# Performance work log

Measured on AMD Instinct MI355X. Metric: run time of the kernel, lower is better.

Reference implementation:

```python
import jax, jax.numpy as jnp
from jax import lax
import numpy as np

B, H, W = 512, 96, 96
KH = KW = 25
PI = 3.141592653589793


def compute_ellipticity(images, counter_target=100, thr=1e-3):
    # images: [B, H, W]
    b, h, w = images.shape
    yv = jnp.arange(h, dtype=jnp.float32) - h / 2.0 + 0.5
    xv = jnp.arange(w, dtype=jnp.float32) - w / 2.0 + 0.5
    Y, X = jnp.meshgrid(yv, xv, indexing='ij')
    X = X[None]  # [1,H,W]
    Y = Y[None]
    area = jnp.float32(h * w)
    total = jnp.sum(images, axis=(1, 2))  # [B]

    init = (jnp.int32(0),
            jnp.full((b,), 3.0, jnp.float32),   # alphax
            jnp.full((b,), 3.0, jnp.float32),   # alphay
            jnp.zeros((b,), jnp.float32),       # alphaxy
            jnp.zeros((b,), jnp.float32),       # mux
            jnp.zeros((b,), jnp.float32),       # muy
            jnp.full((b,), 9999.0, jnp.float32),  # prev_sigxx
            jnp.full((b,), 9999.0, jnp.float32),  # prev_sigyy
            jnp.zeros((b,), jnp.float32),       # curr_sigxx
            jnp.zeros((b,), jnp.float32),       # curr_sigyy
            jnp.zeros((b,), jnp.float32),       # back
            jnp.zeros((b,), jnp.float32),       # e1
            jnp.zeros((b,), jnp.float32))       # e2

    def cond(c):
        i, ax, ay, axy, mux, muy, psxx, psyy, csxx, csyy, back, e1, e2 = c
        first = i == 0
        conv = ((jnp.max(jnp.abs(csxx - psxx)) < thr)
                & (jnp.max(jnp.abs(csyy - psyy)) < thr)
                & jnp.logical_not(first))
        return (i < counter_target) & (first | jnp.logical_not(conv))

    def body(c):
        i, ax, ay, axy, mux, muy, psxx, psyy, csxx, csyy, back, e1, e2 = c
        Xc = X - mux[:, None, None]
        Yc = Y - muy[:, None, None]
        rho = jnp.clip(axy / (ax * ay + 1e-10), -0.99, 0.99)
        arb = jnp.maximum(2.0 * (1.0 - rho ** 2), 1e-10)
        A = 1.0 / (2.0 * PI * ax * ay * jnp.sqrt(1.0 - rho ** 2))
        exp_term = (Xc ** 2 / (arb * ax ** 2)[:, None, None]
                    + Yc ** 2 / (arb * ay ** 2)[:, None, None]
                    - 2.0 * axy[:, None, None] * Xc * Yc
                    / (arb * ax ** 2 * ay ** 2)[:, None, None])
        k = A[:, None, None] * jnp.exp(-jnp.clip(exp_term, 0.0, 50.0))
        img1 = images - back[:, None, None]
        wk = img1 * k
        t1 = jnp.sum(X * Y * wk, axis=(1, 2))
        t2 = jnp.sum(wk, axis=(1, 2))
        t3 = jnp.sum(X * wk, axis=(1, 2))
        t4 = jnp.sum(Y * wk, axis=(1, 2))
        t5 = jnp.sum(X * X * wk, axis=(1, 2))
        t6 = jnp.sum(Y * Y * wk, axis=(1, 2))
        t7 = jnp.sum(k * k, axis=(1, 2))
        flux = t2 / (t7 + 1e-10)
        new_back = (total - flux) / area
        t2s = jnp.maximum(t2, 1e-10)
        new_mux = t3 / t2s
        new_muy = t4 / t2s
        sigxx = t5 / t2s - (t3 / t2s) ** 2
        sigyy = t6 / t2s - (t4 / t2s) ** 2
        sigxy = t1 / t2s - t3 * t4 / (t2s * t2s)
        new_ax = jnp.sqrt(jnp.clip(sigxx * 2.0, 0.81, 100.0))
        new_ay = jnp.sqrt(jnp.clip(sigyy * 2.0, 0.81, 100.0))
        new_axy = 2.0 * sigxy
        den = sigxx + sigyy + 1e-10
        new_e1 = jnp.clip((sigxx - sigyy) / den, -0.99, 0.99)
        new_e2 = jnp.clip(2.0 * sigxy / den, -0.99, 0.99)
        return (i + 1, new_ax, new_ay, new_axy, new_mux, new_muy,
                csxx, csyy, sigxx, sigyy, new_back, new_e1, new_e2)

    final = lax.while_loop(cond, body, init)
    e1, e2 = final[11], final[12]
    e1 = jnp.where(jnp.isnan(e1), 0.0, e1)
    e2 = jnp.where(jnp.isnan(e2), 0.0, e2)
    return e1, e2


def blur_with_kernel(image, kernel):
    # image: [B,H,W,1], kernel: [B,kH,kW,1]; per-sample normalized SAME conv.
    b, h, w, _ = image.shape
    ker = kernel / (jnp.sum(kernel, axis=(1, 2, 3), keepdims=True) + 1e-6)
    img = jnp.transpose(image, (0, 3, 1, 2)).reshape(1, b, h, w)  # batch -> channels
    k = jnp.transpose(ker, (0, 3, 1, 2))                          # [B,1,kH,kW] OIHW
    out = lax.conv_general_dilated(
        img, k, window_strides=(1, 1), padding='SAME',
        feature_group_count=b,
        dimension_numbers=('NCHW', 'OIHW', 'NCHW'))
    return out.reshape(b, 1, h, w).transpose(0, 2, 3, 1)


def percentile_per_sample(t, q):
    # per-sample percentile over axes [1,2,3], keepdims, gather-by-round index
    b = t.shape[0]
    flat = t.reshape(b, -1)
    n = flat.shape[-1]
    kidx = int(round(q / 100.0 * (n - 1)))
    s = jnp.sort(flat, axis=-1)
    return s[:, kidx].reshape(b, 1, 1, 1)


def loss_fn(blurred_img, kernel_img, weight_map, y_true, y_pred):
    weighted_mse = jnp.mean(jnp.square(y_pred - y_true) * weight_map)
    e1_t, e2_t = compute_ellipticity(jnp.squeeze(y_true, -1))
    e1_p, e2_p = compute_ellipticity(jnp.squeeze(y_pred, -1))
    ellip_loss = jnp.mean((e1_t - e1_p) ** 2 + (e2_t - e2_p) ** 2)
    reblurred_raw = blur_with_kernel(y_pred, kernel_img)
    vmin = percentile_per_sample(blurred_img, 1.0)
    vmax = percentile_per_sample(blurred_img, 99.0)
    scale = vmax - vmin + 1e-6
    reblurred = jnp.clip((reblurred_raw - vmin) / scale, 0.0, 2.0)
    reblur_loss = jnp.mean(jnp.square(reblurred - blurred_img) * weight_map)
    total_loss = 100.0 * weighted_mse + 10.0 * reblur_loss
    return total_loss, weighted_mse, ellip_loss, reblur_loss


def setup_inputs() -> dict:
    key = jax.random.key(0)
    ks = jax.random.split(key, 5)
    return {
        'blurred_img': jax.random.uniform(ks[0], (B, H, W, 1), jnp.float32),
        'kernel_img': jax.random.uniform(ks[1], (B, KH, KW, 1), jnp.float32),
        'weight_map': jax.random.uniform(ks[2], (B, H, W, 1), jnp.float32),
        'y_true': jax.random.uniform(ks[3], (B, H, W, 1), jnp.float32),
        'y_pred': jax.random.uniform(ks[4], (B, H, W, 1), jnp.float32),
    }


def reference(blurred_img, kernel_img, weight_map, y_true, y_pred):
    return loss_fn(blurred_img, kernel_img, weight_map, y_true, y_pred)
```

## Files before the change

kernel.cpp:

```cpp
#include <hip/hip_runtime.h>

typedef unsigned int uint32;

#define HW 9216
#define NBATCH 512
#define NPAIR 1024
#define NITER 100
#define TWO_PI_F 6.28318530717958647692f


__device__ __forceinline__ float block_reduce_sum(float v, float* lds) {
#pragma unroll
  for (int m = 1; m < 64; m <<= 1) v += __shfl_xor(v, m, 64);
  __syncthreads();
  if ((threadIdx.x & 63) == 0) lds[threadIdx.x >> 6] = v;
  __syncthreads();
  if (threadIdx.x == 0) {
    int nw = blockDim.x >> 6;
    for (int w = 1; w < nw; ++w) v += lds[w];
  }
  return v;
}


__global__ void init_kernel(double* acc) {
  if (threadIdx.x < 2) acc[threadIdx.x] = 0.0;
}


__global__ void totals_kernel(const float* __restrict__ yt, const float* __restrict__ yp,
                              float* __restrict__ totals) {
  __shared__ float lds[4];
  int pair = blockIdx.x;
  const float* img = (pair < NBATCH) ? (yt + (size_t)pair * HW)
                                     : (yp + (size_t)(pair - NBATCH) * HW);
  float s = 0.f;
  for (int j = threadIdx.x; j < HW; j += 256) s += img[j];
  s = block_reduce_sum(s, lds);
  if (threadIdx.x == 0) totals[pair] = s;
}


__device__ float radix_select(const float* __restrict__ img, int rank,
                              uint32* bins, uint32* selb) {
  uint32 prefix = 0;
  int r = rank;
#pragma unroll 1
  for (int pass = 0; pass < 4; ++pass) {
    int shift = 24 - 8 * pass;
    uint32 maskhi = (pass == 0) ? 0u : (0xFFFFFFFFu << (shift + 8));
    bins[threadIdx.x] = 0;
    __syncthreads();
    for (int j = 0; j < 36; ++j) {
      int px = threadIdx.x + j * 256;
      uint32 bits = __float_as_uint(img[px]);
      uint32 key = (bits & 0x80000000u) ? ~bits : (bits | 0x80000000u);
      if ((key & maskhi) == prefix)
        atomicAdd(&bins[(key >> shift) & 255u], 1u);
    }
    __syncthreads();
    uint32 c = bins[threadIdx.x];
    for (int d = 1; d < 256; d <<= 1) {
      uint32 v = (threadIdx.x >= (unsigned)d) ? bins[threadIdx.x - d] : 0u;
      __syncthreads();
      bins[threadIdx.x] += v;
      __syncthreads();
    }
    uint32 inc = bins[threadIdx.x];
    if (inc > (uint32)r && (inc - c) <= (uint32)r) {
      selb[0] = threadIdx.x;
      selb[1] = (uint32)r - (inc - c);
    }
    __syncthreads();
    prefix |= (selb[0] << shift);
    r = (int)selb[1];
    __syncthreads();
  }
  uint32 key = prefix;
  uint32 bits = (key & 0x80000000u) ? (key ^ 0x80000000u) : ~key;
  return __uint_as_float(bits);
}

__global__ void percentile_kernel(const float* __restrict__ blurred,
                                  float* __restrict__ vmin, float* __restrict__ vmax) {
  __shared__ uint32 bins[256];
  __shared__ uint32 selb[2];
  int b = blockIdx.x;
  const float* img = blurred + (size_t)b * HW;
  float lo = radix_select(img, 92, bins, selb);
  float hi = radix_select(img, 9123, bins, selb);
  if (threadIdx.x == 0) { vmin[b] = lo; vmax[b] = hi; }
}


__global__ void wmse_kernel(const float4* __restrict__ yt, const float4* __restrict__ yp,
                            const float4* __restrict__ wm, double* acc) {
  __shared__ float lds[4];
  int idx = blockIdx.x * 256 + threadIdx.x;
  int stride = gridDim.x * 256;
  float s = 0.f;
  for (int i = idx; i < (NBATCH * HW / 4); i += stride) {
    float4 a = yp[i], b = yt[i], w = wm[i];
    float d;
    d = a.x - b.x; s = fmaf(d * d, w.x, s);
    d = a.y - b.y; s = fmaf(d * d, w.y, s);
    d = a.z - b.z; s = fmaf(d * d, w.z, s);
    d = a.w - b.w; s = fmaf(d * d, w.w, s);
  }
  s = block_reduce_sum(s, lds);
  if (threadIdx.x == 0) atomicAdd(&acc[0], (double)s);
}


__device__ __forceinline__ void accum_row(float* a, const float fr[28], const float* krow) {
  float kv[28];
#pragma unroll
  for (int q = 0; q < 7; ++q) {
    float4 t = *reinterpret_cast<const float4*>(krow + 4 * q);
    kv[4 * q + 0] = t.x; kv[4 * q + 1] = t.y; kv[4 * q + 2] = t.z; kv[4 * q + 3] = t.w;
  }
#pragma unroll
  for (int dx = 0; dx < 25; ++dx) {
    a[0] = fmaf(fr[dx + 0], kv[dx], a[0]);
    a[1] = fmaf(fr[dx + 1], kv[dx], a[1]);
    a[2] = fmaf(fr[dx + 2], kv[dx], a[2]);
    a[3] = fmaf(fr[dx + 3], kv[dx], a[3]);
  }
}

__global__ __launch_bounds__(256, 2) void conv_kernel(
    const float* __restrict__ yp, const float* __restrict__ ker,
    const float* __restrict__ blurred, const float* __restrict__ wmap,
    const float* __restrict__ vminA, const float* __restrict__ vmaxA,
    double* acc) {
  __shared__ float pad[120 * 120];
  __shared__ float kr[25 * 28];
  __shared__ float lds[4];
  __shared__ float sInv;
  int b = blockIdx.x, tid = threadIdx.x;

  const float* kg = ker + (size_t)b * 625;
  float ks = 0.f;
  for (int i = tid; i < 700; i += 256) {
    int r = i / 28, c = i - r * 28;
    float v = (c < 25) ? kg[r * 25 + c] : 0.f;
    kr[i] = v;
    ks += v;
  }
  float ksum = block_reduce_sum(ks, lds);
  if (tid == 0) sInv = 1.f / (ksum + 1e-6f);

  const float* ig = yp + (size_t)b * HW;
  for (int i = tid; i < 14400; i += 256) {
    int r = i / 120, c = i - r * 120;
    float v = 0.f;
    if (r >= 12 && r < 108 && c >= 12 && c < 108) v = ig[(r - 12) * 96 + (c - 12)];
    pad[i] = v;
  }
  __syncthreads();

  float inv = sInv;
  float vmn = vminA[b], vmx = vmaxA[b];
  float scale = vmx - vmn + 1e-6f;
  const float* bl = blurred + (size_t)b * HW;
  const float* wm = wmap + (size_t)b * HW;

  float part = 0.f;
#pragma unroll 1
  for (int t3 = 0; t3 < 3; ++t3) {
    int tile = tid + t3 * 256;
    int ty = tile / 24, tx = tile - ty * 24;
    int y0 = ty * 3, x0 = tx * 4;
    float a0[4] = {0, 0, 0, 0}, a1[4] = {0, 0, 0, 0}, a2[4] = {0, 0, 0, 0};
#pragma unroll 1
    for (int ir = 0; ir < 27; ++ir) {
      float fr[28];
      const float* rp = &pad[(y0 + ir) * 120 + x0];
#pragma unroll
      for (int q = 0; q < 7; ++q) {
        float4 t = *reinterpret_cast<const float4*>(rp + 4 * q);
        fr[4 * q + 0] = t.x; fr[4 * q + 1] = t.y; fr[4 * q + 2] = t.z; fr[4 * q + 3] = t.w;
      }
      if (ir <= 24)            accum_row(a0, fr, &kr[ir * 28]);
      if (ir >= 1 && ir <= 25) accum_row(a1, fr, &kr[(ir - 1) * 28]);
      if (ir >= 2)             accum_row(a2, fr, &kr[(ir - 2) * 28]);
    }
    {
      const float* aa = a0;
#pragma unroll
      for (int r = 0; r < 3; ++r) {
        aa = (r == 0) ? a0 : ((r == 1) ? a1 : a2);
#pragma unroll
        for (int j = 0; j < 4; ++j) {
          int px = (y0 + r) * 96 + x0 + j;
          float raw = aa[j] * inv;
          float rb2 = fminf(fmaxf((raw - vmn) / scale, 0.f), 2.f);
          float d = rb2 - bl[px];
          part = fmaf(d * d, wm[px], part);
        }
      }
    }
  }
  part = block_reduce_sum(part, lds);
  if (tid == 0) atomicAdd(&acc[1], (double)part);
}


__global__ __launch_bounds__(256, 4) void ellipA_kernel(
    const float* __restrict__ yt, const float* __restrict__ yp,
    const float* __restrict__ totals,
    float* __restrict__ dxx, float* __restrict__ dyy,
    float* __restrict__ e1a, float* __restrict__ e2a) {
  const int pair = blockIdx.x;
  const int tid = threadIdx.x;
  const float* img = (pair < NBATCH) ? (yt + (size_t)pair * HW)
                                     : (yp + (size_t)(pair - NBATCH) * HW);
  float im[36];
#pragma unroll
  for (int j = 0; j < 36; ++j) im[j] = img[tid + j * 256];

  __shared__ float bc[8];
  __shared__ float rbuf[28];
  __shared__ int sfroz;

  float ax = 3.f, ay = 3.f, axy = 0.f, mux = 0.f, muy = 0.f, back = 0.f;
  float psxx = 0.f, psyy = 0.f;
  float total = 0.f;
  if (tid == 0) {
    total = totals[pair];
    sfroz = 0;
    float rho = fminf(fmaxf(axy / (ax * ay + 1e-10f), -0.99f), 0.99f);
    float arb = fmaxf(2.f * (1.f - rho * rho), 1e-10f);
    float Ac = 1.f / (TWO_PI_F * ax * ay * sqrtf(1.f - rho * rho));
    bc[0] = mux; bc[1] = muy; bc[2] = back; bc[3] = Ac;
    bc[4] = 1.f / (arb * ax * ax);
    bc[5] = 1.f / (arb * ay * ay);
    bc[6] = -2.f * axy / (arb * ax * ax * ay * ay);
  }
  __syncthreads();

#pragma unroll 1
  for (int n = 0; n < NITER; ++n) {
    float bmux = bc[0], bmuy = bc[1], bback = bc[2], Ac = bc[3];
    float c1 = bc[4], c2 = bc[5], c3 = bc[6];
    float s0 = 0, sx = 0, sy = 0, sxx = 0, syy = 0, sxy = 0, s7 = 0;
    int x = tid % 96, y = tid / 96;
#pragma unroll
    for (int j = 0; j < 36; ++j) {
      float Xc = ((float)x - 47.5f) - bmux;
      float Yc = ((float)y - 47.5f) - bmuy;
      float xc2 = Xc * Xc, yc2 = Yc * Yc, xy = Xc * Yc;
      float t = fmaf(c1, xc2, fmaf(c2, yc2, c3 * xy));
      t = fminf(fmaxf(t, 0.f), 50.f);
      float e = __expf(-t);
      float ge = (im[j] - bback) * e;
      s0 += ge;
      sx = fmaf(Xc, ge, sx);
      sy = fmaf(Yc, ge, sy);
      sxx = fmaf(xc2, ge, sxx);
      syy = fmaf(yc2, ge, syy);
      sxy = fmaf(xy, ge, sxy);
      s7 = fmaf(e, e, s7);
      x += 64;
      if (x >= 96) { x -= 96; y += 3; } else { y += 2; }
    }
#pragma unroll
    for (int m = 1; m < 64; m <<= 1) {
      s0 += __shfl_xor(s0, m, 64);  sx += __shfl_xor(sx, m, 64);
      sy += __shfl_xor(sy, m, 64);  sxx += __shfl_xor(sxx, m, 64);
      syy += __shfl_xor(syy, m, 64); sxy += __shfl_xor(sxy, m, 64);
      s7 += __shfl_xor(s7, m, 64);
    }
    if ((tid & 63) == 0) {
      float* p = &rbuf[(tid >> 6) * 7];
      p[0] = s0; p[1] = sx; p[2] = sy; p[3] = sxx; p[4] = syy; p[5] = sxy; p[6] = s7;
    }
    __syncthreads();
    if (tid == 0) {
      for (int w2 = 1; w2 < 4; ++w2) {
        const float* p = &rbuf[w2 * 7];
        s0 += p[0]; sx += p[1]; sy += p[2]; sxx += p[3]; syy += p[4]; sxy += p[5]; s7 += p[6];
      }
      float t2 = Ac * s0;
      float t3 = Ac * fmaf(bmux, s0, sx);
      float t4 = Ac * fmaf(bmuy, s0, sy);
      float t5 = Ac * (sxx + 2.f * bmux * sx + bmux * bmux * s0);
      float t6 = Ac * (syy + 2.f * bmuy * sy + bmuy * bmuy * s0);
      float t1 = Ac * (sxy + bmux * sy + bmuy * sx + bmux * bmuy * s0);
      float t7 = Ac * Ac * s7;
      float flux = t2 / (t7 + 1e-10f);
      float back_n = (total - flux) / 9216.f;
      float t2s = fmaxf(t2, 1e-10f);
      float mux_n = t3 / t2s, muy_n = t4 / t2s;
      float sigxx = t5 / t2s - mux_n * mux_n;
      float sigyy = t6 / t2s - muy_n * muy_n;
      float sigxy = t1 / t2s - (t3 * t4) / (t2s * t2s);
      float ax_n = sqrtf(fminf(fmaxf(sigxx * 2.f, 0.81f), 100.f));
      float ay_n = sqrtf(fminf(fmaxf(sigyy * 2.f, 0.81f), 100.f));
      float axy_n = 2.f * sigxy;
      float den = sigxx + sigyy + 1e-10f;
      float e1 = fminf(fmaxf((sigxx - sigyy) / den, -0.99f), 0.99f);
      float e2 = fminf(fmaxf((2.f * sigxy) / den, -0.99f), 0.99f);
      float dx_v = fabsf(sigxx - psxx);
      float dy_v = fabsf(sigyy - psyy);
      if (!(dx_v == dx_v)) dx_v = __int_as_float(0x7f800000);
      if (!(dy_v == dy_v)) dy_v = __int_as_float(0x7f800000);
      dxx[n * NPAIR + pair] = dx_v;
      dyy[n * NPAIR + pair] = dy_v;
      e1a[n * NPAIR + pair] = e1;
      e2a[n * NPAIR + pair] = e2;
      bool froz = (ax_n == ax) && (ay_n == ay) && (axy_n == axy) &&
                  (mux_n == mux) && (muy_n == muy) && (back_n == back) &&
                  (dx_v == 0.f) && (dy_v == 0.f);
      psxx = sigxx; psyy = sigyy;
      ax = ax_n; ay = ay_n; axy = axy_n; mux = mux_n; muy = muy_n; back = back_n;
      if (froz) {
        for (int m2 = n + 1; m2 < NITER; ++m2) {
          dxx[m2 * NPAIR + pair] = 0.f;
          dyy[m2 * NPAIR + pair] = 0.f;
          e1a[m2 * NPAIR + pair] = e1;
          e2a[m2 * NPAIR + pair] = e2;
        }
        sfroz = 1;
      } else {
        float rho = fminf(fmaxf(axy / (ax * ay + 1e-10f), -0.99f), 0.99f);
        float arb = fmaxf(2.f * (1.f - rho * rho), 1e-10f);
        float Ac2 = 1.f / (TWO_PI_F * ax * ay * sqrtf(1.f - rho * rho));
        bc[0] = mux; bc[1] = muy; bc[2] = back; bc[3] = Ac2;
        bc[4] = 1.f / (arb * ax * ax);
        bc[5] = 1.f / (arb * ay * ay);
        bc[6] = -2.f * axy / (arb * ax * ax * ay * ay);
      }
    }
    __syncthreads();
    if (sfroz) break;
  }
}


__global__ void ellipB_kernel(const float* __restrict__ dxx, const float* __restrict__ dyy,
                              const float* __restrict__ e1a, const float* __restrict__ e2a,
                              float* __restrict__ out_ellip) {
  __shared__ float rb[8];
  __shared__ int found;
  __shared__ int eidx_sh[2];
  __shared__ float lds[4];
  const int tid = threadIdx.x;

  for (int s = 0; s < 2; ++s) {
    if (tid == 0) { eidx_sh[s] = NITER - 1; found = 0; }
    __syncthreads();
#pragma unroll 1
    for (int n = 0; n < NITER - 1; ++n) {
      int base = n * NPAIR + s * NBATCH;
      float m1 = fmaxf(dxx[base + tid], dxx[base + tid + 256]);
      float m2 = fmaxf(dyy[base + tid], dyy[base + tid + 256]);
#pragma unroll
      for (int m = 1; m < 64; m <<= 1) {
        m1 = fmaxf(m1, __shfl_xor(m1, m, 64));
        m2 = fmaxf(m2, __shfl_xor(m2, m, 64));
      }
      if ((tid & 63) == 0) { rb[(tid >> 6) * 2] = m1; rb[(tid >> 6) * 2 + 1] = m2; }
      __syncthreads();
      if (tid == 0) {
        float M1 = fmaxf(fmaxf(rb[0], rb[2]), fmaxf(rb[4], rb[6]));
        float M2 = fmaxf(fmaxf(rb[1], rb[3]), fmaxf(rb[5], rb[7]));
        if (M1 < 1e-3f && M2 < 1e-3f) { eidx_sh[s] = n; found = 1; }
      }
      __syncthreads();
      if (found) break;
    }
    __syncthreads();
  }

  int i0 = eidx_sh[0], i1 = eidx_sh[1];
  float part = 0.f;
  for (int b = tid; b < NBATCH; b += 256) {
    float e1t = e1a[i0 * NPAIR + b];
    float e2t = e2a[i0 * NPAIR + b];
    float e1p = e1a[i1 * NPAIR + NBATCH + b];
    float e2p = e2a[i1 * NPAIR + NBATCH + b];
    if (!(e1t == e1t)) e1t = 0.f;
    if (!(e2t == e2t)) e2t = 0.f;
    if (!(e1p == e1p)) e1p = 0.f;
    if (!(e2p == e2p)) e2p = 0.f;
    float d1 = e1t - e1p, d2 = e2t - e2p;
    part += d1 * d1 + d2 * d2;
  }
  part = block_reduce_sum(part, lds);
  if (tid == 0) out_ellip[0] = part / (float)NBATCH;
}


__global__ void final_kernel(const double* acc, const float* ellip, float* out) {
  if (threadIdx.x == 0) {
    const double N = 4718592.0;
    float wm = (float)(acc[0] / N);
    float rb = (float)(acc[1] / N);
    out[0] = 100.f * wm + 10.f * rb;
    out[1] = wm;
    out[2] = ellip[0];
    out[3] = rb;
  }
}


extern "C" void kernel_launch(void* const* d_in, const int* in_sizes, int n_in,
                              void* d_out, int out_size, void* d_ws, size_t ws_size,
                              hipStream_t stream) {
  const float* blurred = (const float*)d_in[0];
  const float* kernel_img = (const float*)d_in[1];
  const float* wmap = (const float*)d_in[2];
  const float* y_true = (const float*)d_in[3];
  const float* y_pred = (const float*)d_in[4];
  float* out = (float*)d_out;

  double* acc = (double*)d_ws;
  float* wsf = (float*)d_ws;
  float* ellip = wsf + 4;
  float* vmin = wsf + 8;
  float* vmax = vmin + NBATCH;
  float* totals = vmax + NBATCH;
  float* dxx = totals + NPAIR;
  float* dyy = dxx + NITER * NPAIR;
  float* e1a = dyy + NITER * NPAIR;
  float* e2a = e1a + NITER * NPAIR;

  init_kernel<<<1, 64, 0, stream>>>(acc);
  totals_kernel<<<NPAIR, 256, 0, stream>>>(y_true, y_pred, totals);
  percentile_kernel<<<NBATCH, 256, 0, stream>>>(blurred, vmin, vmax);
  wmse_kernel<<<1024, 256, 0, stream>>>((const float4*)y_true, (const float4*)y_pred,
                                        (const float4*)wmap, acc);
  conv_kernel<<<NBATCH, 256, 0, stream>>>(y_pred, kernel_img, blurred, wmap, vmin, vmax, acc);
  ellipA_kernel<<<NPAIR, 256, 0, stream>>>(y_true, y_pred, totals, dxx, dyy, e1a, e2a);
  ellipB_kernel<<<1, 256, 0, stream>>>(dxx, dyy, e1a, e2a, ellip);
  final_kernel<<<1, 64, 0, stream>>>(acc, ellip, out);
}
```

Measured before the change: 1.198 ms.

## Fuse image totals into ellipse kernel and replicate per-iteration scalar update

Removes the separate totals kernel and computes each image's sum inside the ellipse-fitting kernel from the registers it already loaded. The per-iteration scalar update, previously done by thread 0 and broadcast through shared memory with a second barrier, is now computed redundantly by every thread from double-buffered wave partials, so each iteration needs one barrier instead of two. The per-iteration output arrays move to a pair-major layout to match the new writes, and the reduction kernel is updated for that layout. In exchange, every thread does the scalar math with divisions and sqrt, and the reduction kernel's reads become strided.

```diff
diff --git a/kernel.cpp b/kernel.cpp
--- a/kernel.cpp
+++ b/kernel.cpp
@@ -25,19 +25,6 @@
 
 __global__ void init_kernel(double* acc) {
   if (threadIdx.x < 2) acc[threadIdx.x] = 0.0;
-}
-
-
-__global__ void totals_kernel(const float* __restrict__ yt, const float* __restrict__ yp,
-                              float* __restrict__ totals) {
-  __shared__ float lds[4];
-  int pair = blockIdx.x;
-  const float* img = (pair < NBATCH) ? (yt + (size_t)pair * HW)
-                                     : (yp + (size_t)(pair - NBATCH) * HW);
-  float s = 0.f;
-  for (int j = threadIdx.x; j < HW; j += 256) s += img[j];
-  s = block_reduce_sum(s, lds);
-  if (threadIdx.x == 0) totals[pair] = s;
 }
 
 
@@ -208,7 +195,6 @@
 
 __global__ __launch_bounds__(256, 4) void ellipA_kernel(
     const float* __restrict__ yt, const float* __restrict__ yp,
-    const float* __restrict__ totals,
     float* __restrict__ dxx, float* __restrict__ dyy,
     float* __restrict__ e1a, float* __restrict__ e2a) {
   const int pair = blockIdx.x;
@@ -219,30 +205,38 @@
 #pragma unroll
   for (int j = 0; j < 36; ++j) im[j] = img[tid + j * 256];
 
-  __shared__ float bc[8];
-  __shared__ float rbuf[28];
-  __shared__ int sfroz;
+  __shared__ float rbuf[2][4][8];
+  __shared__ float tbuf[4];
+
+  {
+    float t = 0.f;
+#pragma unroll
+    for (int j = 0; j < 36; ++j) t += im[j];
+#pragma unroll
+    for (int m = 1; m < 64; m <<= 1) t += __shfl_xor(t, m, 64);
+    if ((tid & 63) == 0) tbuf[tid >> 6] = t;
+  }
+  __syncthreads();
+  const float total = ((tbuf[0] + tbuf[1]) + tbuf[2]) + tbuf[3];
 
   float ax = 3.f, ay = 3.f, axy = 0.f, mux = 0.f, muy = 0.f, back = 0.f;
   float psxx = 0.f, psyy = 0.f;
-  float total = 0.f;
-  if (tid == 0) {
-    total = totals[pair];
-    sfroz = 0;
+
+  float* dxx_p = dxx + (size_t)pair * NITER;
+  float* dyy_p = dyy + (size_t)pair * NITER;
+  float* e1_p = e1a + (size_t)pair * NITER;
+  float* e2_p = e2a + (size_t)pair * NITER;
+
+#pragma unroll 1
+  for (int n = 0; n < NITER; ++n) {
     float rho = fminf(fmaxf(axy / (ax * ay + 1e-10f), -0.99f), 0.99f);
     float arb = fmaxf(2.f * (1.f - rho * rho), 1e-10f);
     float Ac = 1.f / (TWO_PI_F * ax * ay * sqrtf(1.f - rho * rho));
-    bc[0] = mux; bc[1] = muy; bc[2] = back; bc[3] = Ac;
-    bc[4] = 1.f / (arb * ax * ax);
-    bc[5] = 1.f / (arb * ay * ay);
-    bc[6] = -2.f * axy / (arb * ax * ax * ay * ay);
-  }
-  __syncthreads();
-
-#pragma unroll 1
-  for (int n = 0; n < NITER; ++n) {
-    float bmux = bc[0], bmuy = bc[1], bback = bc[2], Ac = bc[3];
-    float c1 = bc[4], c2 = bc[5], c3 = bc[6];
+    float c1 = 1.f / (arb * ax * ax);
+    float c2 = 1.f / (arb * ay * ay);
+    float c3 = -2.f * axy / (arb * ax * ax * ay * ay);
+    float bmux = mux, bmuy = muy, bback = back;
+
     float s0 = 0, sx = 0, sy = 0, sxx = 0, syy = 0, sxy = 0, s7 = 0;
     int x = tid % 96, y = tid / 96;
 #pragma unroll
@@ -271,69 +265,64 @@
       syy += __shfl_xor(syy, m, 64); sxy += __shfl_xor(sxy, m, 64);
       s7 += __shfl_xor(s7, m, 64);
     }
+    int buf = n & 1;
     if ((tid & 63) == 0) {
-      float* p = &rbuf[(tid >> 6) * 7];
+      float* p = &rbuf[buf][tid >> 6][0];
       p[0] = s0; p[1] = sx; p[2] = sy; p[3] = sxx; p[4] = syy; p[5] = sxy; p[6] = s7;
     }
     __syncthreads();
+    {
+      const float* p0 = &rbuf[buf][0][0];
+      const float* p1 = &rbuf[buf][1][0];
+      const float* p2 = &rbuf[buf][2][0];
+      const float* p3 = &rbuf[buf][3][0];
+      s0 = ((p0[0] + p1[0]) + p2[0]) + p3[0];
+      sx = ((p0[1] + p1[1]) + p2[1]) + p3[1];
+      sy = ((p0[2] + p1[2]) + p2[2]) + p3[2];
+      sxx = ((p0[3] + p1[3]) + p2[3]) + p3[3];
+      syy = ((p0[4] + p1[4]) + p2[4]) + p3[4];
+      sxy = ((p0[5] + p1[5]) + p2[5]) + p3[5];
+      s7 = ((p0[6] + p1[6]) + p2[6]) + p3[6];
+    }
+
+    float t2 = Ac * s0;
+    float t3 = Ac * fmaf(bmux, s0, sx);
+    float t4 = Ac * fmaf(bmuy, s0, sy);
+    float t5 = Ac * (sxx + 2.f * bmux * sx + bmux * bmux * s0);
+    float t6 = Ac * (syy + 2.f * bmuy * sy + bmuy * bmuy * s0);
+    float t1 = Ac * (sxy + bmux * sy + bmuy * sx + bmux * bmuy * s0);
+    float t7 = Ac * Ac * s7;
+    float flux = t2 / (t7 + 1e-10f);
+    float back_n = (total - flux) / 9216.f;
+    float t2s = fmaxf(t2, 1e-10f);
+    float mux_n = t3 / t2s, muy_n = t4 / t2s;
+    float sigxx = t5 / t2s - mux_n * mux_n;
+    float sigyy = t6 / t2s - muy_n * muy_n;
+    float sigxy = t1 / t2s - (t3 * t4) / (t2s * t2s);
+    float ax_n = sqrtf(fminf(fmaxf(sigxx * 2.f, 0.81f), 100.f));
+    float ay_n = sqrtf(fminf(fmaxf(sigyy * 2.f, 0.81f), 100.f));
+    float axy_n = 2.f * sigxy;
+    float den = sigxx + sigyy + 1e-10f;
+    float e1 = fminf(fmaxf((sigxx - sigyy) / den, -0.99f), 0.99f);
+    float e2 = fminf(fmaxf((2.f * sigxy) / den, -0.99f), 0.99f);
+    float dx_v = fabsf(sigxx - psxx);
+    float dy_v = fabsf(sigyy - psyy);
+    if (!(dx_v == dx_v)) dx_v = __int_as_float(0x7f800000);
+    if (!(dy_v == dy_v)) dy_v = __int_as_float(0x7f800000);
     if (tid == 0) {
-      for (int w2 = 1; w2 < 4; ++w2) {
-        const float* p = &rbuf[w2 * 7];
-        s0 += p[0]; sx += p[1]; sy += p[2]; sxx += p[3]; syy += p[4]; sxy += p[5]; s7 += p[6];
+      dxx_p[n] = dx_v; dyy_p[n] = dy_v; e1_p[n] = e1; e2_p[n] = e2;
+    }
+    bool froz = (ax_n == ax) && (ay_n == ay) && (axy_n == axy) &&
+                (mux_n == mux) && (muy_n == muy) && (back_n == back) &&
+                (dx_v == 0.f) && (dy_v == 0.f);
+    psxx = sigxx; psyy = sigyy;
+    ax = ax_n; ay = ay_n; axy = axy_n; mux = mux_n; muy = muy_n; back = back_n;
+    if (froz) {
+      for (int m2 = n + 1 + tid; m2 < NITER; m2 += 256) {
+        dxx_p[m2] = 0.f; dyy_p[m2] = 0.f; e1_p[m2] = e1; e2_p[m2] = e2;
       }
-      float t2 = Ac * s0;
-      float t3 = Ac * fmaf(bmux, s0, sx);
-      float t4 = Ac * fmaf(bmuy, s0, sy);
-      float t5 = Ac * (sxx + 2.f * bmux * sx + bmux * bmux * s0);
-      float t6 = Ac * (syy + 2.f * bmuy * sy + bmuy * bmuy * s0);
-      float t1 = Ac * (sxy + bmux * sy + bmuy * sx + bmux * bmuy * s0);
-      float t7 = Ac * Ac * s7;
-      float flux = t2 / (t7 + 1e-10f);
-      float back_n = (total - flux) / 9216.f;
-      float t2s = fmaxf(t2, 1e-10f);
-      float mux_n = t3 / t2s, muy_n = t4 / t2s;
-      float sigxx = t5 / t2s - mux_n * mux_n;
-      float sigyy = t6 / t2s - muy_n * muy_n;
-      float sigxy = t1 / t2s - (t3 * t4) / (t2s * t2s);
-      float ax_n = sqrtf(fminf(fmaxf(sigxx * 2.f, 0.81f), 100.f));
-      float ay_n = sqrtf(fminf(fmaxf(sigyy * 2.f, 0.81f), 100.f));
-      float axy_n = 2.f * sigxy;
-      float den = sigxx + sigyy + 1e-10f;
-      float e1 = fminf(fmaxf((sigxx - sigyy) / den, -0.99f), 0.99f);
-      float e2 = fminf(fmaxf((2.f * sigxy) / den, -0.99f), 0.99f);
-      float dx_v = fabsf(sigxx - psxx);
-      float dy_v = fabsf(sigyy - psyy);
-      if (!(dx_v == dx_v)) dx_v = __int_as_float(0x7f800000);
-      if (!(dy_v == dy_v)) dy_v = __int_as_float(0x7f800000);
-      dxx[n * NPAIR + pair] = dx_v;
-      dyy[n * NPAIR + pair] = dy_v;
-      e1a[n * NPAIR + pair] = e1;
-      e2a[n * NPAIR + pair] = e2;
-      bool froz = (ax_n == ax) && (ay_n == ay) && (axy_n == axy) &&
-                  (mux_n == mux) && (muy_n == muy) && (back_n == back) &&
-                  (dx_v == 0.f) && (dy_v == 0.f);
-      psxx = sigxx; psyy = sigyy;
-      ax = ax_n; ay = ay_n; axy = axy_n; mux = mux_n; muy = muy_n; back = back_n;
-      if (froz) {
-        for (int m2 = n + 1; m2 < NITER; ++m2) {
-          dxx[m2 * NPAIR + pair] = 0.f;
-          dyy[m2 * NPAIR + pair] = 0.f;
-          e1a[m2 * NPAIR + pair] = e1;
-          e2a[m2 * NPAIR + pair] = e2;
-        }
-        sfroz = 1;
-      } else {
-        float rho = fminf(fmaxf(axy / (ax * ay + 1e-10f), -0.99f), 0.99f);
-        float arb = fmaxf(2.f * (1.f - rho * rho), 1e-10f);
-        float Ac2 = 1.f / (TWO_PI_F * ax * ay * sqrtf(1.f - rho * rho));
-        bc[0] = mux; bc[1] = muy; bc[2] = back; bc[3] = Ac2;
-        bc[4] = 1.f / (arb * ax * ax);
-        bc[5] = 1.f / (arb * ay * ay);
-        bc[6] = -2.f * axy / (arb * ax * ax * ay * ay);
-      }
-    }
-    __syncthreads();
-    if (sfroz) break;
+      break;
+    }
   }
 }
 
@@ -352,9 +341,10 @@
     __syncthreads();
 #pragma unroll 1
     for (int n = 0; n < NITER - 1; ++n) {
-      int base = n * NPAIR + s * NBATCH;
-      float m1 = fmaxf(dxx[base + tid], dxx[base + tid + 256]);
-      float m2 = fmaxf(dyy[base + tid], dyy[base + tid + 256]);
+      size_t i0 = (size_t)(s * NBATCH + tid) * NITER + n;
+      size_t i1 = (size_t)(s * NBATCH + tid + 256) * NITER + n;
+      float m1 = fmaxf(dxx[i0], dxx[i1]);
+      float m2 = fmaxf(dyy[i0], dyy[i1]);
 #pragma unroll
       for (int m = 1; m < 64; m <<= 1) {
         m1 = fmaxf(m1, __shfl_xor(m1, m, 64));
@@ -376,10 +366,10 @@
   int i0 = eidx_sh[0], i1 = eidx_sh[1];
   float part = 0.f;
   for (int b = tid; b < NBATCH; b += 256) {
-    float e1t = e1a[i0 * NPAIR + b];
-    float e2t = e2a[i0 * NPAIR + b];
-    float e1p = e1a[i1 * NPAIR + NBATCH + b];
-    float e2p = e2a[i1 * NPAIR + NBATCH + b];
+    float e1t = e1a[(size_t)b * NITER + i0];
+    float e2t = e2a[(size_t)b * NITER + i0];
+    float e1p = e1a[(size_t)(NBATCH + b) * NITER + i1];
+    float e2p = e2a[(size_t)(NBATCH + b) * NITER + i1];
     if (!(e1t == e1t)) e1t = 0.f;
     if (!(e2t == e2t)) e2t = 0.f;
     if (!(e1p == e1p)) e1p = 0.f;
@@ -420,19 +410,17 @@
   float* ellip = wsf + 4;
   float* vmin = wsf + 8;
   float* vmax = vmin + NBATCH;
-  float* totals = vmax + NBATCH;
-  float* dxx = totals + NPAIR;
+  float* dxx = vmax + NBATCH;
   float* dyy = dxx + NITER * NPAIR;
   float* e1a = dyy + NITER * NPAIR;
   float* e2a = e1a + NITER * NPAIR;
 
   init_kernel<<<1, 64, 0, stream>>>(acc);
-  totals_kernel<<<NPAIR, 256, 0, stream>>>(y_true, y_pred, totals);
   percentile_kernel<<<NBATCH, 256, 0, stream>>>(blurred, vmin, vmax);
   wmse_kernel<<<1024, 256, 0, stream>>>((const float4*)y_true, (const float4*)y_pred,
                                         (const float4*)wmap, acc);
   conv_kernel<<<NBATCH, 256, 0, stream>>>(y_pred, kernel_img, blurred, wmap, vmin, vmax, acc);
-  ellipA_kernel<<<NPAIR, 256, 0, stream>>>(y_true, y_pred, totals, dxx, dyy, e1a, e2a);
+  ellipA_kernel<<<NPAIR, 256, 0, stream>>>(y_true, y_pred, dxx, dyy, e1a, e2a);
   ellipB_kernel<<<1, 256, 0, stream>>>(dxx, dyy, e1a, e2a, ellip);
   final_kernel<<<1, 64, 0, stream>>>(acc, ellip, out);
 }
```

Result: slower. 2.253 ms (+88.1%).
